# Kernel optimization log

Measured on AMD Instinct MI355X. Metric: run time of the kernel, lower is better.

The kernel has to match this reference:

```python
import jax, jax.numpy as jnp
import numpy as np

HEADS = 16
GN_EPS = 1e-5
NEG = -1e30  # finite stand-in for -inf to keep softmax/vjp NaN-free


def setup_inputs() -> dict:
    key = jax.random.key(0)
    k0, k1, k2, k3 = jax.random.split(key, 4)
    B, C, T = 8, 1024, 1024
    x = jax.random.normal(k0, (B, C, T), dtype=jnp.float32)
    mask = jax.random.randint(k1, (B, T), 0, 2).astype(bool)  # True = masked position
    w_kvq = jax.random.normal(k2, (3 * C, C), dtype=jnp.float32) * 0.02  # Conv1d k=1 == per-time GEMM
    w_out = jax.random.normal(k3, (C, C), dtype=jnp.float32) * 0.02
    gn_weight = jnp.ones((C,), dtype=jnp.float32)
    gn_bias = jnp.zeros((C,), dtype=jnp.float32)
    return {"x": x, "mask": mask, "w_kvq": w_kvq, "w_out": w_out,
            "gn_weight": gn_weight, "gn_bias": gn_bias}


def reference(x, mask, w_kvq, w_out, gn_weight, gn_bias):
    B, C, T = x.shape
    H = HEADS
    d = C // H
    # QKV projection (1x1 conv == GEMM over channels)
    kvq = jnp.einsum('oc,bct->bot', w_kvq, x)  # [B, 3C, T]
    k = kvq[:, :C].reshape(B, H, d, T)
    v = kvq[:, C:2 * C].reshape(B, H, d, T)
    q = kvq[:, 2 * C:].reshape(B, H, d, T)
    scale = 1.0 / np.sqrt(d).astype(np.float32)
    # att[b,h,k,q] = <k_k, q_q> / sqrt(d)
    att = jnp.einsum('bhdk,bhdq->bhkq', k, q) * scale
    # mask key rows, softmax over key axis, then zero masked query columns
    att = jnp.where(mask[:, None, :, None], NEG, att)
    att = jax.nn.softmax(att, axis=2)
    att = jnp.where(mask[:, None, None, :], 0.0, att)
    ctx = jnp.einsum('bhdk,bhkq->bhdq', v, att).reshape(B, C, T)
    out = jnp.einsum('oc,bct->bot', w_out, ctx)
    y = out + x  # residual
    # GroupNorm(1, C): normalize over (C, T) per sample, per-channel affine
    mean = jnp.mean(y, axis=(1, 2), keepdims=True)
    var = jnp.var(y, axis=(1, 2), keepdims=True)
    y = (y - mean) * jax.lax.rsqrt(var + GN_EPS)
    y = y * gn_weight[None, :, None] + gn_bias[None, :, None]
    # torch layout of returned attention: chunks over heads concatenated on batch dim
    att_ret = att.transpose(1, 0, 2, 3).reshape(H * B, T, T)
    return y, att_ret
```

## Files before the change

kernel.cpp:

```cpp
#include <hip/hip_runtime.h>

#define DEVI __device__ __forceinline__

typedef __attribute__((ext_vector_type(8))) short s16x8;
typedef __attribute__((ext_vector_type(4))) float f32x4;
typedef __attribute__((ext_vector_type(4))) unsigned short u16x4;
typedef __attribute__((ext_vector_type(4))) int i32x4;

static constexpr int NB = 8;
static constexpr int NC = 1024;
static constexpr int NT = 1024;
static constexpr int NH = 16;
static constexpr int ND = 64;

DEVI unsigned short cvt_bf16(float f) {
  unsigned int u = __builtin_bit_cast(unsigned int, f);
  u += 0x7fffu + ((u >> 16) & 1u);
  return (unsigned short)(u >> 16);
}

DEVI float fexp2(float x) {
#if __has_builtin(__builtin_amdgcn_exp2f)
  return __builtin_amdgcn_exp2f(x);
#else
  return exp2f(x);
#endif
}

template<int ROWS>
DEVI void stage_tile(const unsigned short* g, int ld, char* lds, int loff, int tid) {
  const int wave = tid >> 6;
  const int lane = tid & 63;
#pragma unroll
  for (int r = 0; r < (ROWS >> 5); ++r) {
    const int row = r * 32 + wave * 8 + (lane >> 3);
    const int c  = lane & 7;
    const int cg = c ^ (row & 7);
    const char* src = (const char*)g + (size_t)row * ld * 2 + cg * 16;
    char* dst = lds + loff + (r * 32 + wave * 8) * 128;
    __builtin_amdgcn_global_load_lds((const __attribute__((address_space(1))) void*)src,
                                     (__attribute__((address_space(3))) void*)dst,
                                     16, 0, 0);
  }
}

DEVI void stage_v(const unsigned short* v, int k0, char* lds, int loff, int tid) {
  const int wave = tid >> 6;
  const int lane = tid & 63;
#pragma unroll
  for (int it = 0; it < 4; ++it) {
    const int d = wave * 16 + it * 4 + (lane >> 4);
    const int c = lane & 15;
    const int cg = c ^ (d & 15);
    const char* src = (const char*)(v + (size_t)d * NT + k0 + cg * 8);
    char* dst = lds + loff + (wave * 16 + it * 4) * 256;
    __builtin_amdgcn_global_load_lds((const __attribute__((address_space(1))) void*)src,
                                     (__attribute__((address_space(3))) void*)dst,
                                     16, 0, 0);
  }
}

DEVI s16x8 frag_ld(const char* lds, int loff, int row, int ks, int lane) {
  const int chunk = (ks * 4 + (lane >> 4)) ^ (row & 7);
  return *(const s16x8*)(lds + loff + row * 128 + chunk * 16);
}

template<int KTOT>
DEVI void gemm_core_128(const unsigned short* A, const unsigned short* Bt,
                        int ldA, int ldB, char* lds, int tid, f32x4 acc[4][4]) {
  const int lane = tid & 63;
  const int wave = tid >> 6;
  const int wr = wave >> 1, wc = wave & 1;
#pragma unroll
  for (int i = 0; i < 4; ++i)
#pragma unroll
    for (int j = 0; j < 4; ++j)
      acc[i][j] = (f32x4){0.f, 0.f, 0.f, 0.f};
  for (int k0 = 0; k0 < KTOT; k0 += 64) {
    __syncthreads();
    stage_tile<128>(A + k0, ldA, lds, 0, tid);
    stage_tile<128>(Bt + k0, ldB, lds, 16384, tid);
    asm volatile("s_waitcnt vmcnt(0)" ::: "memory");
    __syncthreads();
#pragma unroll
    for (int ks = 0; ks < 2; ++ks) {
      s16x8 af[4], bfr[4];
#pragma unroll
      for (int mf = 0; mf < 4; ++mf)
        af[mf] = frag_ld(lds, 0, wr * 64 + mf * 16 + (lane & 15), ks, lane);
#pragma unroll
      for (int nf = 0; nf < 4; ++nf)
        bfr[nf] = frag_ld(lds, 16384, wc * 64 + nf * 16 + (lane & 15), ks, lane);
#pragma unroll
      for (int mf = 0; mf < 4; ++mf)
#pragma unroll
        for (int nf = 0; nf < 4; ++nf)
          acc[mf][nf] = __builtin_amdgcn_mfma_f32_16x16x32_bf16(af[mf], bfr[nf], acc[mf][nf], 0, 0, 0);
    }
  }
}

__global__ __launch_bounds__(256) void k_prep(const float* __restrict__ wkvq,
                                              unsigned short* __restrict__ wkvq_bf,
                                              const float* __restrict__ wout,
                                              unsigned short* __restrict__ wout_bf) {
  const int n1 = 3 * NC * NC / 4, n2 = NC * NC / 4;
  const int stride = gridDim.x * blockDim.x;
  for (int i = blockIdx.x * blockDim.x + threadIdx.x; i < n1 + n2; i += stride) {
    const float* src = (i < n1) ? wkvq + (size_t)i * 4 : wout + (size_t)(i - n1) * 4;
    unsigned short* dst = (i < n1) ? wkvq_bf + (size_t)i * 4 : wout_bf + (size_t)(i - n1) * 4;
    f32x4 v = *(const f32x4*)src;
    u16x4 o;
#pragma unroll
    for (int j = 0; j < 4; ++j) o[j] = cvt_bf16(v[j]);
    *(u16x4*)dst = o;
  }
}

__global__ void k_xT(const float* __restrict__ x, unsigned short* __restrict__ xT) {
  __shared__ float tl[32][33];
  const int bz = blockIdx.z;
  const int t0 = blockIdx.x * 32, c0 = blockIdx.y * 32;
  const int tx = threadIdx.x, ty = threadIdx.y;
#pragma unroll
  for (int j = 0; j < 4; ++j)
    tl[ty + j * 8][tx] = x[((size_t)bz * NC + c0 + ty + j * 8) * NT + t0 + tx];
  __syncthreads();
#pragma unroll
  for (int j = 0; j < 4; ++j)
    xT[((size_t)bz * NT + t0 + ty + j * 8) * NC + c0 + tx] = cvt_bf16(tl[tx][ty + j * 8]);
}

__global__ __launch_bounds__(512, 2) void k_gemm1_256(const unsigned short* __restrict__ W,
                                                      const unsigned short* __restrict__ xT,
                                                      unsigned short* __restrict__ kt,
                                                      unsigned short* __restrict__ qt,
                                                      unsigned short* __restrict__ vbuf) {
  __shared__ char lds[131072];
  const int tid = threadIdx.x, lane = tid & 63, wid = tid >> 6;
  const int wr = wid >> 2, wc = wid & 3;
  const int gid = blockIdx.x;
  const int wg = (gid & 7) * 48 + (gid >> 3);
  const int bn = wg / 12, bm = wg % 12;

  const int r = tid >> 2, ccc = tid & 3;
  const int cg = ccc ^ ((r ^ (r >> 2)) & 3);
  const unsigned short* srcA = W + (size_t)(bm * 256 + r) * NC + cg * 8;
  const unsigned short* srcB = xT + (size_t)(bn * 256 + r) * NC + cg * 8;

  auto stageA = [&](int t) {
    char* d = lds + (t & 3) * 32768 + wid * 1024;
    const unsigned short* s = srcA + t * 32;
    __builtin_amdgcn_global_load_lds((const __attribute__((address_space(1))) void*)s,
                                     (__attribute__((address_space(3))) void*)d, 16, 0, 0);
    __builtin_amdgcn_global_load_lds((const __attribute__((address_space(1))) void*)(s + 128 * NC),
                                     (__attribute__((address_space(3))) void*)(d + 8192), 16, 0, 0);
  };
  auto stageB = [&](int t) {
    char* d = lds + (t & 3) * 32768 + 16384 + wid * 1024;
    const unsigned short* s = srcB + t * 32;
    __builtin_amdgcn_global_load_lds((const __attribute__((address_space(1))) void*)s,
                                     (__attribute__((address_space(3))) void*)d, 16, 0, 0);
    __builtin_amdgcn_global_load_lds((const __attribute__((address_space(1))) void*)(s + 128 * NC),
                                     (__attribute__((address_space(3))) void*)(d + 8192), 16, 0, 0);
  };

  const int l15 = lane & 15, lg = lane >> 4;
  const int rA = wr * 128 + l15;
  const int offA = rA * 64 + (((lg ^ (rA ^ (rA >> 2))) & 3) << 4) + ((lg & ~3) << 4);
  const int rB = wc * 64 + l15;
  const int offB = 16384 + rB * 64 + (((lg ^ (rB ^ (rB >> 2))) & 3) << 4) + ((lg & ~3) << 4);

  f32x4 acc[8][4];
#pragma unroll
  for (int i = 0; i < 8; ++i)
#pragma unroll
    for (int j = 0; j < 4; ++j) acc[i][j] = (f32x4){0.f, 0.f, 0.f, 0.f};

  stageA(0); stageB(0); stageA(1); stageB(1); stageA(2); stageB(2);
  asm volatile("s_waitcnt vmcnt(8)" ::: "memory");
  __builtin_amdgcn_s_barrier();

#pragma unroll
  for (int t = 0; t < 32; ++t) {
    const int slot = (t & 3) * 32768;
    s16x8 af[8], bf[4];
#pragma unroll
    for (int nf = 0; nf < 4; ++nf) bf[nf] = *(const s16x8*)(lds + slot + offB + nf * 1024);
#pragma unroll
    for (int mf = 0; mf < 4; ++mf) af[mf] = *(const s16x8*)(lds + slot + offA + mf * 1024);
    if (t < 29) stageA(t + 3);
    __builtin_amdgcn_s_barrier();
    asm volatile("s_waitcnt lgkmcnt(0)" ::: "memory");
    __builtin_amdgcn_sched_barrier(0);
    __builtin_amdgcn_s_setprio(1);
#pragma unroll
    for (int mf = 0; mf < 4; ++mf)
#pragma unroll
      for (int nf = 0; nf < 4; ++nf)
        acc[mf][nf] = __builtin_amdgcn_mfma_f32_16x16x32_bf16(af[mf], bf[nf], acc[mf][nf], 0, 0, 0);
    __builtin_amdgcn_s_setprio(0);
    __builtin_amdgcn_s_barrier();
#pragma unroll
    for (int mf = 4; mf < 8; ++mf) af[mf] = *(const s16x8*)(lds + slot + offA + mf * 1024);
    if (t < 29) stageB(t + 3);
    if (t < 29)       asm volatile("s_waitcnt vmcnt(8)" ::: "memory");
    else if (t == 29) asm volatile("s_waitcnt vmcnt(4)" ::: "memory");
    else              asm volatile("s_waitcnt vmcnt(0)" ::: "memory");
    __builtin_amdgcn_s_barrier();
    asm volatile("s_waitcnt lgkmcnt(0)" ::: "memory");
    __builtin_amdgcn_sched_barrier(0);
    __builtin_amdgcn_s_setprio(1);
#pragma unroll
    for (int mf = 4; mf < 8; ++mf)
#pragma unroll
      for (int nf = 0; nf < 4; ++nf)
        acc[mf][nf] = __builtin_amdgcn_mfma_f32_16x16x32_bf16(af[mf], bf[nf], acc[mf][nf], 0, 0, 0);
    __builtin_amdgcn_s_setprio(0);
    __builtin_amdgcn_s_barrier();
  }

  const int part = bm >> 2;
  const int d0base = lg << 2;
#pragma unroll
  for (int mf = 0; mf < 8; ++mf) {
    const int h = ((bm & 3) << 2) + (wr << 1) + (mf >> 2);
    const int d0 = ((mf & 3) << 4) + d0base;
#pragma unroll
    for (int nf = 0; nf < 4; ++nf) {
      const int tg = bn * 256 + wc * 64 + nf * 16 + l15;
      const int b = tg >> 10, tt = tg & 1023;
      u16x4 v4;
#pragma unroll
      for (int i = 0; i < 4; ++i) v4[i] = cvt_bf16(acc[mf][nf][i]);
      if (part == 0) {
        *(u16x4*)(kt + (((size_t)(b * NH + h) * NT + tt) * ND + d0)) = v4;
      } else if (part == 1) {
        const size_t basev = ((size_t)(b * NH + h) * ND + d0) * NT + tt;
        vbuf[basev] = v4[0]; vbuf[basev + NT] = v4[1];
        vbuf[basev + 2 * NT] = v4[2]; vbuf[basev + 3 * NT] = v4[3];
      } else {
        *(u16x4*)(qt + (((size_t)(b * NH + h) * NT + tt) * ND + d0)) = v4;
      }
    }
  }
}

__global__ __launch_bounds__(256, 2) void k_att(const unsigned short* __restrict__ kt,
                                                const unsigned short* __restrict__ qt,
                                                const unsigned short* __restrict__ vbuf,
                                                const int* __restrict__ mask,
                                                float* __restrict__ att,
                                                unsigned short* __restrict__ ctxT) {
  __shared__ char lds[81920];
  constexpr int KOFF = 0, QOFF = 16384, VOFF = 32768, POFF = 49152;
  float* colacc = (float*)(lds + POFF);
  unsigned long long* mbits = (unsigned long long*)(lds + POFF + 512);
  const int tid = threadIdx.x, lane = tid & 63, wave = tid >> 6;
  const int wr = wave >> 1, wc = wave & 1;
  const int bh = blockIdx.x, qb = blockIdx.y;
  const int b = bh >> 4, h = bh & 15, hb = h * NB + b;
  const int q0 = qb * 128;
  const unsigned short* ktp = kt + (size_t)bh * NT * ND;
  const unsigned short* qtp = qt + ((size_t)bh * NT + q0) * ND;
  const unsigned short* vp  = vbuf + (size_t)bh * ND * NT;
  const int l15 = lane & 15, g = lane >> 4;

  if (tid < 128) colacc[tid] = 0.f;
  stage_tile<128>(qtp, ND, lds, QOFF, tid);
#pragma unroll
  for (int j = 0; j < 4; ++j) {
    unsigned long long bb = __ballot(mask[b * NT + wave * 256 + j * 64 + lane] != 0);
    if (lane == 0) mbits[wave * 4 + j] = bb;
  }
  i32x4 qm4[4];
#pragma unroll
  for (int nf = 0; nf < 4; ++nf)
    qm4[nf] = *(const i32x4*)(mask + b * NT + q0 + wc * 64 + nf * 16 + g * 4);
  asm volatile("s_waitcnt vmcnt(0)" ::: "memory");
  __syncthreads();

  s16x8 qf[4][2];
#pragma unroll
  for (int nf = 0; nf < 4; ++nf)
#pragma unroll
    for (int ks = 0; ks < 2; ++ks)
      qf[nf][ks] = frag_ld(lds, QOFF, wc * 64 + nf * 16 + l15, ks, lane);

  unsigned int kmask32 = 0;
#pragma unroll
  for (int t = 0; t < 8; ++t) {
    const unsigned long long w64 = mbits[t * 2 + wr];
#pragma unroll
    for (int mf = 0; mf < 4; ++mf)
      kmask32 |= (unsigned int)((w64 >> (mf * 16 + l15)) & 1ull) << (t * 4 + mf);
  }

  const float scl = 0.125f * 1.44269504f;

  f32x4 cs4[4];
#pragma unroll
  for (int nf = 0; nf < 4; ++nf) cs4[nf] = (f32x4){0.f, 0.f, 0.f, 0.f};
  stage_tile<128>(ktp, ND, lds, KOFF, tid);
  for (int t = 0; t < 8; ++t) {
    __builtin_amdgcn_s_barrier();
    if (t < 7) {
      stage_tile<128>(ktp + (size_t)(t + 1) * 128 * ND, ND, lds, (t & 1) ? KOFF : VOFF, tid);
      asm volatile("s_waitcnt vmcnt(4)" ::: "memory");
    } else {
      asm volatile("s_waitcnt vmcnt(0)" ::: "memory");
    }
    __builtin_amdgcn_s_barrier();
    const int koff = (t & 1) ? VOFF : KOFF;
    f32x4 sacc[4][4];
#pragma unroll
    for (int i = 0; i < 4; ++i)
#pragma unroll
      for (int j = 0; j < 4; ++j) sacc[i][j] = (f32x4){0.f, 0.f, 0.f, 0.f};
#pragma unroll
    for (int ks = 0; ks < 2; ++ks) {
      s16x8 kf[4];
#pragma unroll
      for (int mf = 0; mf < 4; ++mf)
        kf[mf] = frag_ld(lds, koff, wr * 64 + mf * 16 + l15, ks, lane);
#pragma unroll
      for (int mf = 0; mf < 4; ++mf)
#pragma unroll
        for (int nf = 0; nf < 4; ++nf)
          sacc[mf][nf] = __builtin_amdgcn_mfma_f32_16x16x32_bf16(qf[nf][ks], kf[mf], sacc[mf][nf], 0, 0, 0);
    }
#pragma unroll
    for (int mf = 0; mf < 4; ++mf) {
      const float kz = ((kmask32 >> (t * 4 + mf)) & 1u) ? 0.f : 1.f;
#pragma unroll
      for (int nf = 0; nf < 4; ++nf)
#pragma unroll
        for (int i = 0; i < 4; ++i)
          cs4[nf][i] += kz * fexp2(sacc[mf][nf][i] * scl);
    }
  }
#pragma unroll
  for (int nf = 0; nf < 4; ++nf)
#pragma unroll
    for (int i = 0; i < 4; ++i) {
      float v = cs4[nf][i];
      v += __shfl_xor(v, 1); v += __shfl_xor(v, 2);
      v += __shfl_xor(v, 4); v += __shfl_xor(v, 8);
      cs4[nf][i] = v;
    }
  if (l15 == 0) {
#pragma unroll
    for (int nf = 0; nf < 4; ++nf)
#pragma unroll
      for (int i = 0; i < 4; ++i)
        atomicAdd(&colacc[wc * 64 + nf * 16 + g * 4 + i], cs4[nf][i]);
  }
  __syncthreads();
  f32x4 sq4[4];
#pragma unroll
  for (int nf = 0; nf < 4; ++nf)
#pragma unroll
    for (int i = 0; i < 4; ++i)
      sq4[nf][i] = qm4[nf][i] ? 0.f : 1.0f / colacc[wc * 64 + nf * 16 + g * 4 + i];

  f32x4 cacc[4][2];
#pragma unroll
  for (int i = 0; i < 4; ++i)
#pragma unroll
    for (int j = 0; j < 2; ++j) cacc[i][j] = (f32x4){0.f, 0.f, 0.f, 0.f};

  stage_tile<128>(ktp, ND, lds, KOFF, tid);
  stage_v(vp, 0, lds, VOFF, tid);
  asm volatile("s_waitcnt vmcnt(0)" ::: "memory");
  __builtin_amdgcn_s_barrier();

  float* attb = att + (size_t)hb * NT * NT + q0 + wc * 64 + g * 4;
  for (int t = 0; t < 8; ++t) {
    f32x4 sacc[4][4];
#pragma unroll
    for (int i = 0; i < 4; ++i)
#pragma unroll
      for (int j = 0; j < 4; ++j) sacc[i][j] = (f32x4){0.f, 0.f, 0.f, 0.f};
#pragma unroll
    for (int ks = 0; ks < 2; ++ks) {
      s16x8 kf[4];
#pragma unroll
      for (int mf = 0; mf < 4; ++mf)
        kf[mf] = frag_ld(lds, KOFF, wr * 64 + mf * 16 + l15, ks, lane);
#pragma unroll
      for (int mf = 0; mf < 4; ++mf)
#pragma unroll
        for (int nf = 0; nf < 4; ++nf)
          sacc[mf][nf] = __builtin_amdgcn_mfma_f32_16x16x32_bf16(qf[nf][ks], kf[mf], sacc[mf][nf], 0, 0, 0);
    }
    __builtin_amdgcn_s_barrier();
    if (t < 7) stage_tile<128>(ktp + (size_t)(t + 1) * 128 * ND, ND, lds, KOFF, tid);
    __builtin_amdgcn_sched_barrier(0);

#pragma unroll
    for (int mf = 0; mf < 4; ++mf) {
      const int kg = t * 128 + wr * 64 + mf * 16 + l15;
      const float kz = ((kmask32 >> (t * 4 + mf)) & 1u) ? 0.f : 1.f;
      const int kloc = wr * 64 + mf * 16 + l15;
#pragma unroll
      for (int nf = 0; nf < 4; ++nf) {
        f32x4 p4;
#pragma unroll
        for (int i = 0; i < 4; ++i)
          p4[i] = kz * fexp2(sacc[mf][nf][i] * scl) * sq4[nf][i];
        __builtin_nontemporal_store(p4, (f32x4*)(attb + (size_t)kg * NT + nf * 16));
        const int qrow = wc * 64 + nf * 16 + g * 4;
#pragma unroll
        for (int i = 0; i < 4; ++i) {
          const int row = qrow + i;
          *(unsigned short*)(lds + POFF + row * 256 + (((kloc >> 3) ^ (row & 15)) << 4)
                             + ((kloc & 7) << 1)) = cvt_bf16(p4[i]);
        }
      }
    }
    asm volatile("s_waitcnt lgkmcnt(0)" ::: "memory");
    __builtin_amdgcn_sched_barrier(0);
    __builtin_amdgcn_s_barrier();
    if (t > 0) {
      if (t < 7) asm volatile("s_waitcnt vmcnt(20)" ::: "memory");
      else       asm volatile("s_waitcnt vmcnt(16)" ::: "memory");
    }

#pragma unroll
    for (int ks2 = 0; ks2 < 4; ++ks2) {
      s16x8 vf[4], pf[2];
      const int chunk = (ks2 << 2) + g;
#pragma unroll
      for (int mf = 0; mf < 4; ++mf) {
        const int d = mf * 16 + l15;
        vf[mf] = *(const s16x8*)(lds + VOFF + d * 256 + ((chunk ^ (d & 15)) << 4));
      }
#pragma unroll
      for (int nf2 = 0; nf2 < 2; ++nf2) {
        const int qloc = wave * 32 + nf2 * 16 + l15;
        pf[nf2] = *(const s16x8*)(lds + POFF + qloc * 256 + ((chunk ^ (qloc & 15)) << 4));
      }
#pragma unroll
      for (int mf = 0; mf < 4; ++mf)
#pragma unroll
        for (int nf2 = 0; nf2 < 2; ++nf2)
          cacc[mf][nf2] = __builtin_amdgcn_mfma_f32_16x16x32_bf16(vf[mf], pf[nf2], cacc[mf][nf2], 0, 0, 0);
    }
    __builtin_amdgcn_s_barrier();
    if (t < 7) {
      stage_v(vp, (t + 1) * 128, lds, VOFF, tid);
      asm volatile("s_waitcnt vmcnt(20)" ::: "memory");
      __builtin_amdgcn_s_barrier();
    }
  }

#pragma unroll
  for (int mf = 0; mf < 4; ++mf) {
    const int d0 = mf * 16 + (g << 2);
#pragma unroll
    for (int nf2 = 0; nf2 < 2; ++nf2) {
      const int q = q0 + wave * 32 + nf2 * 16 + l15;
      u16x4 v4;
#pragma unroll
      for (int i = 0; i < 4; ++i) v4[i] = cvt_bf16(cacc[mf][nf2][i]);
      *(u16x4*)(ctxT + ((size_t)b * NT + q) * NC + h * ND + d0) = v4;
    }
  }
}

__global__ __launch_bounds__(256) void k_outgemm(const unsigned short* __restrict__ Wo,
                                                 const unsigned short* __restrict__ ctxT,
                                                 const float* __restrict__ x,
                                                 float* __restrict__ y0,
                                                 float* __restrict__ partials) {
  __shared__ char lds[32832];
  const int tid = threadIdx.x, lane = tid & 63, wave = tid >> 6;
  const int wr = wave >> 1, wc = wave & 1;
  const int bm = blockIdx.x, bn = blockIdx.y, b = blockIdx.z;
  const unsigned short* A = Wo + (size_t)bm * 128 * NC;
  const unsigned short* Bt = ctxT + ((size_t)b * NT + (size_t)bn * 128) * NC;
  f32x4 acc[4][4];
  gemm_core_128<NC>(A, Bt, NC, NC, lds, tid, acc);

  float lsum = 0.f, lsq = 0.f;
#pragma unroll
  for (int mf = 0; mf < 4; ++mf) {
#pragma unroll
    for (int nf = 0; nf < 4; ++nf) {
      const int gc = bn * 128 + wc * 64 + nf * 16 + (lane & 15);
#pragma unroll
      for (int i = 0; i < 4; ++i) {
        const int gr = bm * 128 + wr * 64 + mf * 16 + ((lane >> 4) << 2) + i;
        const size_t idx = ((size_t)b * NC + gr) * NT + gc;
        const float v = acc[mf][nf][i] + x[idx];
        y0[idx] = v;
        lsum += v; lsq += v * v;
      }
    }
  }
#pragma unroll
  for (int off = 32; off; off >>= 1) {
    lsum += __shfl_xor(lsum, off);
    lsq += __shfl_xor(lsq, off);
  }
  __syncthreads();
  float* red = (float*)(lds + 32768);
  if (lane == 0) { red[wave * 2] = lsum; red[wave * 2 + 1] = lsq; }
  __syncthreads();
  if (tid == 0) {
    const float s = red[0] + red[2] + red[4] + red[6];
    const float qq = red[1] + red[3] + red[5] + red[7];
    const int bi = bm * 8 + bn;
    partials[((size_t)b * 64 + bi) * 2] = s;
    partials[((size_t)b * 64 + bi) * 2 + 1] = qq;
  }
}

__global__ void k_gnstats(const float* __restrict__ partials, float* __restrict__ gnp) {
  const int b = blockIdx.x, t = threadIdx.x;
  float s = partials[((size_t)b * 64 + t) * 2];
  float q = partials[((size_t)b * 64 + t) * 2 + 1];
#pragma unroll
  for (int off = 32; off; off >>= 1) {
    s += __shfl_xor(s, off);
    q += __shfl_xor(q, off);
  }
  if (t == 0) {
    const float n = 1048576.f;
    const float mean = s / n;
    const float var = q / n - mean * mean;
    gnp[b * 2] = mean;
    gnp[b * 2 + 1] = rsqrtf(var + 1e-5f);
  }
}

__global__ __launch_bounds__(256) void k_gnapply(const float* __restrict__ y0,
                                                 const float* __restrict__ gnp,
                                                 const float* __restrict__ gw,
                                                 const float* __restrict__ gb,
                                                 float* __restrict__ out) {
  const size_t n4 = (size_t)NB * NC * NT / 4;
  const size_t stride = (size_t)gridDim.x * blockDim.x;
  for (size_t i = (size_t)blockIdx.x * blockDim.x + threadIdx.x; i < n4; i += stride) {
    const size_t base = i * 4;
    const int b = (int)(base >> 20);
    const int c = (int)((base >> 10) & 1023);
    const f32x4 v = *(const f32x4*)(y0 + base);
    const float m = gnp[b * 2], r = gnp[b * 2 + 1];
    const float sw = gw[c] * r, sb = gb[c];
    f32x4 o;
#pragma unroll
    for (int j = 0; j < 4; ++j) o[j] = (v[j] - m) * sw + sb;
    *(f32x4*)(out + base) = o;
  }
}

extern "C" void kernel_launch(void* const* d_in, const int* in_sizes, int n_in,
                              void* d_out, int out_size, void* d_ws, size_t ws_size,
                              hipStream_t stream) {
  (void)in_sizes; (void)n_in; (void)out_size; (void)ws_size;
  const float* x     = (const float*)d_in[0];
  const int*   mask  = (const int*)d_in[1];
  const float* w_kvq = (const float*)d_in[2];
  const float* w_out = (const float*)d_in[3];
  const float* gnw   = (const float*)d_in[4];
  const float* gnb   = (const float*)d_in[5];
  float* outy = (float*)d_out;
  float* att  = outy + (size_t)NB * NC * NT;

  char* ws = (char*)d_ws;
  unsigned short* wkvq_bf = (unsigned short*)(ws);
  unsigned short* wout_bf = (unsigned short*)(ws + 6291456);
  unsigned short* xT      = (unsigned short*)(ws + 8388608);
  unsigned short* ctxT    = xT;
  unsigned short* kt      = (unsigned short*)(ws + 25165824);
  unsigned short* qt      = (unsigned short*)(ws + 41943040);
  float*          y0      = (float*)(ws + 25165824);
  unsigned short* vbuf    = (unsigned short*)(ws + 58720256);
  float*          part    = (float*)(ws + 76021760);
  float*          gnp     = (float*)(ws + 76025856);

  k_prep<<<2048, 256, 0, stream>>>(w_kvq, wkvq_bf, w_out, wout_bf);
  k_xT<<<dim3(32, 32, 8), dim3(32, 8), 0, stream>>>(x, xT);
  k_gemm1_256<<<384, 512, 0, stream>>>(wkvq_bf, xT, kt, qt, vbuf);
  k_att<<<dim3(128, 8), 256, 0, stream>>>(kt, qt, vbuf, mask, att, ctxT);
  k_outgemm<<<dim3(8, 8, 8), 256, 0, stream>>>(wout_bf, ctxT, x, y0, part);
  k_gnstats<<<8, 64, 0, stream>>>(part, gnp);
  k_gnapply<<<4096, 256, 0, stream>>>(y0, gnp, gnw, gnb, outy);
}
```

Measured before the change: 346.6 us.

## Single-pass attention: cache unnormalized probabilities in registers, normalize afterward

The attention kernel previously made two passes over K: one to compute column softmax sums and another to recompute QK^T, normalize, write the attention matrix and accumulate P·V. It now makes one pass that computes exp scores, accumulates column sums, stores unnormalized bf16 probabilities in registers and LDS, and accumulates P·V immediately. Normalization is applied afterward to the context and to the cached probabilities written to the attention output. Blocks go from 256 to 512 threads with double-buffered K/V staging, which raises register pressure (64 u16x4 cached per thread) and rounds the stored attention values through bf16.

```diff
diff --git a/kernel.cpp b/kernel.cpp
--- a/kernel.cpp
+++ b/kernel.cpp
@@ -17,6 +17,11 @@
   unsigned int u = __builtin_bit_cast(unsigned int, f);
   u += 0x7fffu + ((u >> 16) & 1u);
   return (unsigned short)(u >> 16);
+}
+
+DEVI float bf16_to_f32(unsigned short s) {
+  unsigned int u = (unsigned int)s << 16;
+  return __builtin_bit_cast(float, u);
 }
 
 DEVI float fexp2(float x) {
@@ -44,16 +49,27 @@
   }
 }
 
-DEVI void stage_v(const unsigned short* v, int k0, char* lds, int loff, int tid) {
-  const int wave = tid >> 6;
-  const int lane = tid & 63;
-#pragma unroll
-  for (int it = 0; it < 4; ++it) {
-    const int d = wave * 16 + it * 4 + (lane >> 4);
-    const int c = lane & 15;
-    const int cg = c ^ (d & 15);
+DEVI void stage_k512(const unsigned short* g, char* lds, int loff, int tid) {
+  const int wave = tid >> 6, lane = tid & 63;
+#pragma unroll
+  for (int r = 0; r < 2; ++r) {
+    const int row = r * 64 + wave * 8 + (lane >> 3);
+    const int c = lane & 7, cg = c ^ (row & 7);
+    const char* src = (const char*)g + (size_t)row * 128 + cg * 16;
+    char* dst = lds + loff + (r * 64 + wave * 8) * 128;
+    __builtin_amdgcn_global_load_lds((const __attribute__((address_space(1))) void*)src,
+                                     (__attribute__((address_space(3))) void*)dst,
+                                     16, 0, 0);
+  }
+}
+DEVI void stage_v512(const unsigned short* v, int k0, char* lds, int loff, int tid) {
+  const int wave = tid >> 6, lane = tid & 63;
+#pragma unroll
+  for (int r = 0; r < 2; ++r) {
+    const int d = r * 32 + wave * 4 + (lane >> 4);
+    const int c = lane & 15, cg = c ^ (d & 15);
     const char* src = (const char*)(v + (size_t)d * NT + k0 + cg * 8);
-    char* dst = lds + loff + (wave * 16 + it * 4) * 256;
+    char* dst = lds + loff + (r * 32 + wave * 4) * 256;
     __builtin_amdgcn_global_load_lds((const __attribute__((address_space(1))) void*)src,
                                      (__attribute__((address_space(3))) void*)dst,
                                      16, 0, 0);
@@ -246,18 +262,19 @@
   }
 }
 
-__global__ __launch_bounds__(256, 2) void k_att(const unsigned short* __restrict__ kt,
-                                                const unsigned short* __restrict__ qt,
-                                                const unsigned short* __restrict__ vbuf,
-                                                const int* __restrict__ mask,
-                                                float* __restrict__ att,
-                                                unsigned short* __restrict__ ctxT) {
-  __shared__ char lds[81920];
-  constexpr int KOFF = 0, QOFF = 16384, VOFF = 32768, POFF = 49152;
-  float* colacc = (float*)(lds + POFF);
-  unsigned long long* mbits = (unsigned long long*)(lds + POFF + 512);
-  const int tid = threadIdx.x, lane = tid & 63, wave = tid >> 6;
-  const int wr = wave >> 1, wc = wave & 1;
+__global__ __launch_bounds__(512, 1) void k_att2(const unsigned short* __restrict__ kt,
+                                                 const unsigned short* __restrict__ qt,
+                                                 const unsigned short* __restrict__ vbuf,
+                                                 const int* __restrict__ mask,
+                                                 float* __restrict__ att,
+                                                 unsigned short* __restrict__ ctxT) {
+  __shared__ char lds[115456];
+  constexpr int QOFF = 0, KOFF0 = 16384, KOFF1 = 32768, VOFF0 = 49152, VOFF1 = 65536;
+  constexpr int POFF = 81920, COFF = 114688;
+  float* colacc = (float*)(lds + COFF);
+  unsigned long long* mbits = (unsigned long long*)(lds + COFF + 512);
+  const int tid = threadIdx.x, lane = tid & 63, wid = tid >> 6;
+  const int wr = wid >> 2, wc = wid & 3;
   const int bh = blockIdx.x, qb = blockIdx.y;
   const int b = bh >> 4, h = bh & 15, hb = h * NB + b;
   const int q0 = qb * 128;
@@ -267,25 +284,27 @@
   const int l15 = lane & 15, g = lane >> 4;
 
   if (tid < 128) colacc[tid] = 0.f;
-  stage_tile<128>(qtp, ND, lds, QOFF, tid);
-#pragma unroll
-  for (int j = 0; j < 4; ++j) {
-    unsigned long long bb = __ballot(mask[b * NT + wave * 256 + j * 64 + lane] != 0);
-    if (lane == 0) mbits[wave * 4 + j] = bb;
-  }
-  i32x4 qm4[4];
-#pragma unroll
-  for (int nf = 0; nf < 4; ++nf)
-    qm4[nf] = *(const i32x4*)(mask + b * NT + q0 + wc * 64 + nf * 16 + g * 4);
+  stage_k512(qtp, lds, QOFF, tid);
+  stage_k512(ktp, lds, KOFF0, tid);
+  stage_v512(vp, 0, lds, VOFF0, tid);
+#pragma unroll
+  for (int j = 0; j < 2; ++j) {
+    unsigned long long bb = __ballot(mask[b * NT + wid * 128 + j * 64 + lane] != 0);
+    if (lane == 0) mbits[wid * 2 + j] = bb;
+  }
+  i32x4 qm4[2];
+#pragma unroll
+  for (int nf = 0; nf < 2; ++nf)
+    qm4[nf] = *(const i32x4*)(mask + b * NT + q0 + wc * 32 + nf * 16 + g * 4);
   asm volatile("s_waitcnt vmcnt(0)" ::: "memory");
   __syncthreads();
 
-  s16x8 qf[4][2];
-#pragma unroll
-  for (int nf = 0; nf < 4; ++nf)
+  s16x8 qf[2][2];
+#pragma unroll
+  for (int nf = 0; nf < 2; ++nf)
 #pragma unroll
     for (int ks = 0; ks < 2; ++ks)
-      qf[nf][ks] = frag_ld(lds, QOFF, wc * 64 + nf * 16 + l15, ks, lane);
+      qf[nf][ks] = frag_ld(lds, QOFF, wc * 32 + nf * 16 + l15, ks, lane);
 
   unsigned int kmask32 = 0;
 #pragma unroll
@@ -297,26 +316,31 @@
   }
 
   const float scl = 0.125f * 1.44269504f;
-
-  f32x4 cs4[4];
-#pragma unroll
-  for (int nf = 0; nf < 4; ++nf) cs4[nf] = (f32x4){0.f, 0.f, 0.f, 0.f};
-  stage_tile<128>(ktp, ND, lds, KOFF, tid);
+  u16x4 preg[8][8];
+  f32x4 cs4[2] = {(f32x4){0.f,0.f,0.f,0.f}, (f32x4){0.f,0.f,0.f,0.f}};
+  f32x4 cacc[4];
+#pragma unroll
+  for (int i = 0; i < 4; ++i) cacc[i] = (f32x4){0.f, 0.f, 0.f, 0.f};
+
+#pragma unroll
   for (int t = 0; t < 8; ++t) {
-    __builtin_amdgcn_s_barrier();
+    if (t > 0) __builtin_amdgcn_s_barrier();
     if (t < 7) {
-      stage_tile<128>(ktp + (size_t)(t + 1) * 128 * ND, ND, lds, (t & 1) ? KOFF : VOFF, tid);
+      stage_k512(ktp + (size_t)(t + 1) * 128 * ND, lds, (t & 1) ? KOFF0 : KOFF1, tid);
+      stage_v512(vp, (t + 1) * 128, lds, (t & 1) ? VOFF0 : VOFF1, tid);
       asm volatile("s_waitcnt vmcnt(4)" ::: "memory");
     } else {
       asm volatile("s_waitcnt vmcnt(0)" ::: "memory");
     }
     __builtin_amdgcn_s_barrier();
-    const int koff = (t & 1) ? VOFF : KOFF;
-    f32x4 sacc[4][4];
+    const int koff = (t & 1) ? KOFF1 : KOFF0;
+    const int voff = (t & 1) ? VOFF1 : VOFF0;
+
+    f32x4 sacc[4][2];
 #pragma unroll
     for (int i = 0; i < 4; ++i)
 #pragma unroll
-      for (int j = 0; j < 4; ++j) sacc[i][j] = (f32x4){0.f, 0.f, 0.f, 0.f};
+      for (int j = 0; j < 2; ++j) sacc[i][j] = (f32x4){0.f, 0.f, 0.f, 0.f};
 #pragma unroll
     for (int ks = 0; ks < 2; ++ks) {
       s16x8 kf[4];
@@ -326,21 +350,58 @@
 #pragma unroll
       for (int mf = 0; mf < 4; ++mf)
 #pragma unroll
-        for (int nf = 0; nf < 4; ++nf)
+        for (int nf = 0; nf < 2; ++nf)
           sacc[mf][nf] = __builtin_amdgcn_mfma_f32_16x16x32_bf16(qf[nf][ks], kf[mf], sacc[mf][nf], 0, 0, 0);
     }
+
 #pragma unroll
     for (int mf = 0; mf < 4; ++mf) {
       const float kz = ((kmask32 >> (t * 4 + mf)) & 1u) ? 0.f : 1.f;
-#pragma unroll
-      for (int nf = 0; nf < 4; ++nf)
-#pragma unroll
-        for (int i = 0; i < 4; ++i)
-          cs4[nf][i] += kz * fexp2(sacc[mf][nf][i] * scl);
-    }
-  }
-#pragma unroll
-  for (int nf = 0; nf < 4; ++nf)
+      const int kloc = wr * 64 + mf * 16 + l15;
+#pragma unroll
+      for (int nf = 0; nf < 2; ++nf) {
+        f32x4 p;
+#pragma unroll
+        for (int i = 0; i < 4; ++i) {
+          p[i] = kz * fexp2(sacc[mf][nf][i] * scl);
+          cs4[nf][i] += p[i];
+        }
+        u16x4 pr;
+#pragma unroll
+        for (int i = 0; i < 4; ++i) pr[i] = cvt_bf16(p[i]);
+        preg[t][mf * 2 + nf] = pr;
+        const int qrow = wc * 32 + nf * 16 + g * 4;
+#pragma unroll
+        for (int i = 0; i < 4; ++i) {
+          const int row = qrow + i;
+          *(unsigned short*)(lds + POFF + row * 256 + (((kloc >> 3) ^ (row & 15)) << 4)
+                             + ((kloc & 7) << 1)) = pr[i];
+        }
+      }
+    }
+    asm volatile("s_waitcnt lgkmcnt(0)" ::: "memory");
+    __builtin_amdgcn_sched_barrier(0);
+    __builtin_amdgcn_s_barrier();
+
+#pragma unroll
+    for (int ks2 = 0; ks2 < 4; ++ks2) {
+      const int chunk = (ks2 << 2) + g;
+      s16x8 vf[4];
+#pragma unroll
+      for (int mf = 0; mf < 4; ++mf) {
+        const int d = mf * 16 + l15;
+        vf[mf] = *(const s16x8*)(lds + voff + d * 256 + ((chunk ^ (d & 15)) << 4));
+      }
+      const int qloc = wid * 16 + l15;
+      s16x8 pf = *(const s16x8*)(lds + POFF + qloc * 256 + ((chunk ^ (qloc & 15)) << 4));
+#pragma unroll
+      for (int mf = 0; mf < 4; ++mf)
+        cacc[mf] = __builtin_amdgcn_mfma_f32_16x16x32_bf16(vf[mf], pf, cacc[mf], 0, 0, 0);
+    }
+  }
+
+#pragma unroll
+  for (int nf = 0; nf < 2; ++nf)
 #pragma unroll
     for (int i = 0; i < 4; ++i) {
       float v = cs4[nf][i];
@@ -350,120 +411,45 @@
     }
   if (l15 == 0) {
 #pragma unroll
-    for (int nf = 0; nf < 4; ++nf)
+    for (int nf = 0; nf < 2; ++nf)
 #pragma unroll
       for (int i = 0; i < 4; ++i)
-        atomicAdd(&colacc[wc * 64 + nf * 16 + g * 4 + i], cs4[nf][i]);
+        atomicAdd(&colacc[wc * 32 + nf * 16 + g * 4 + i], cs4[nf][i]);
   }
   __syncthreads();
-  f32x4 sq4[4];
-#pragma unroll
-  for (int nf = 0; nf < 4; ++nf)
+  f32x4 sq4[2];
+#pragma unroll
+  for (int nf = 0; nf < 2; ++nf)
 #pragma unroll
     for (int i = 0; i < 4; ++i)
-      sq4[nf][i] = qm4[nf][i] ? 0.f : 1.0f / colacc[wc * 64 + nf * 16 + g * 4 + i];
-
-  f32x4 cacc[4][2];
-#pragma unroll
-  for (int i = 0; i < 4; ++i)
-#pragma unroll
-    for (int j = 0; j < 2; ++j) cacc[i][j] = (f32x4){0.f, 0.f, 0.f, 0.f};
-
-  stage_tile<128>(ktp, ND, lds, KOFF, tid);
-  stage_v(vp, 0, lds, VOFF, tid);
-  asm volatile("s_waitcnt vmcnt(0)" ::: "memory");
-  __builtin_amdgcn_s_barrier();
-
-  float* attb = att + (size_t)hb * NT * NT + q0 + wc * 64 + g * 4;
+      sq4[nf][i] = qm4[nf][i] ? 0.f : 1.0f / colacc[wc * 32 + nf * 16 + g * 4 + i];
+
+  {
+    const int qe = wid * 16 + l15;
+    const float sqe = mask[b * NT + q0 + qe] ? 0.f : 1.0f / colacc[qe];
+#pragma unroll
+    for (int mf = 0; mf < 4; ++mf) {
+      u16x4 v4;
+#pragma unroll
+      for (int i = 0; i < 4; ++i) v4[i] = cvt_bf16(cacc[mf][i] * sqe);
+      *(u16x4*)(ctxT + ((size_t)b * NT + q0 + qe) * NC + h * ND + mf * 16 + g * 4) = v4;
+    }
+  }
+
+  float* attb = att + (size_t)hb * NT * NT + q0 + wc * 32 + g * 4;
+#pragma unroll
   for (int t = 0; t < 8; ++t) {
-    f32x4 sacc[4][4];
-#pragma unroll
-    for (int i = 0; i < 4; ++i)
-#pragma unroll
-      for (int j = 0; j < 4; ++j) sacc[i][j] = (f32x4){0.f, 0.f, 0.f, 0.f};
-#pragma unroll
-    for (int ks = 0; ks < 2; ++ks) {
-      s16x8 kf[4];
-#pragma unroll
-      for (int mf = 0; mf < 4; ++mf)
-        kf[mf] = frag_ld(lds, KOFF, wr * 64 + mf * 16 + l15, ks, lane);
-#pragma unroll
-      for (int mf = 0; mf < 4; ++mf)
-#pragma unroll
-        for (int nf = 0; nf < 4; ++nf)
-          sacc[mf][nf] = __builtin_amdgcn_mfma_f32_16x16x32_bf16(qf[nf][ks], kf[mf], sacc[mf][nf], 0, 0, 0);
-    }
-    __builtin_amdgcn_s_barrier();
-    if (t < 7) stage_tile<128>(ktp + (size_t)(t + 1) * 128 * ND, ND, lds, KOFF, tid);
-    __builtin_amdgcn_sched_barrier(0);
-
 #pragma unroll
     for (int mf = 0; mf < 4; ++mf) {
       const int kg = t * 128 + wr * 64 + mf * 16 + l15;
-      const float kz = ((kmask32 >> (t * 4 + mf)) & 1u) ? 0.f : 1.f;
-      const int kloc = wr * 64 + mf * 16 + l15;
-#pragma unroll
-      for (int nf = 0; nf < 4; ++nf) {
+#pragma unroll
+      for (int nf = 0; nf < 2; ++nf) {
+        const u16x4 pr = preg[t][mf * 2 + nf];
         f32x4 p4;
 #pragma unroll
-        for (int i = 0; i < 4; ++i)
-          p4[i] = kz * fexp2(sacc[mf][nf][i] * scl) * sq4[nf][i];
+        for (int i = 0; i < 4; ++i) p4[i] = bf16_to_f32(pr[i]) * sq4[nf][i];
         __builtin_nontemporal_store(p4, (f32x4*)(attb + (size_t)kg * NT + nf * 16));
-        const int qrow = wc * 64 + nf * 16 + g * 4;
-#pragma unroll
-        for (int i = 0; i < 4; ++i) {
-          const int row = qrow + i;
-          *(unsigned short*)(lds + POFF + row * 256 + (((kloc >> 3) ^ (row & 15)) << 4)
-                             + ((kloc & 7) << 1)) = cvt_bf16(p4[i]);
-        }
       }
-    }
-    asm volatile("s_waitcnt lgkmcnt(0)" ::: "memory");
-    __builtin_amdgcn_sched_barrier(0);
-    __builtin_amdgcn_s_barrier();
-    if (t > 0) {
-      if (t < 7) asm volatile("s_waitcnt vmcnt(20)" ::: "memory");
-      else       asm volatile("s_waitcnt vmcnt(16)" ::: "memory");
-    }
-
-#pragma unroll
-    for (int ks2 = 0; ks2 < 4; ++ks2) {
-      s16x8 vf[4], pf[2];
-      const int chunk = (ks2 << 2) + g;
-#pragma unroll
-      for (int mf = 0; mf < 4; ++mf) {
-        const int d = mf * 16 + l15;
-        vf[mf] = *(const s16x8*)(lds + VOFF + d * 256 + ((chunk ^ (d & 15)) << 4));
-      }
-#pragma unroll
-      for (int nf2 = 0; nf2 < 2; ++nf2) {
-        const int qloc = wave * 32 + nf2 * 16 + l15;
-        pf[nf2] = *(const s16x8*)(lds + POFF + qloc * 256 + ((chunk ^ (qloc & 15)) << 4));
-      }
-#pragma unroll
-      for (int mf = 0; mf < 4; ++mf)
-#pragma unroll
-        for (int nf2 = 0; nf2 < 2; ++nf2)
-          cacc[mf][nf2] = __builtin_amdgcn_mfma_f32_16x16x32_bf16(vf[mf], pf[nf2], cacc[mf][nf2], 0, 0, 0);
-    }
-    __builtin_amdgcn_s_barrier();
-    if (t < 7) {
-      stage_v(vp, (t + 1) * 128, lds, VOFF, tid);
-      asm volatile("s_waitcnt vmcnt(20)" ::: "memory");
-      __builtin_amdgcn_s_barrier();
-    }
-  }
-
-#pragma unroll
-  for (int mf = 0; mf < 4; ++mf) {
-    const int d0 = mf * 16 + (g << 2);
-#pragma unroll
-    for (int nf2 = 0; nf2 < 2; ++nf2) {
-      const int q = q0 + wave * 32 + nf2 * 16 + l15;
-      u16x4 v4;
-#pragma unroll
-      for (int i = 0; i < 4; ++i) v4[i] = cvt_bf16(cacc[mf][nf2][i]);
-      *(u16x4*)(ctxT + ((size_t)b * NT + q) * NC + h * ND + d0) = v4;
     }
   }
 }
@@ -583,7 +569,7 @@
   k_prep<<<2048, 256, 0, stream>>>(w_kvq, wkvq_bf, w_out, wout_bf);
   k_xT<<<dim3(32, 32, 8), dim3(32, 8), 0, stream>>>(x, xT);
   k_gemm1_256<<<384, 512, 0, stream>>>(wkvq_bf, xT, kt, qt, vbuf);
-  k_att<<<dim3(128, 8), 256, 0, stream>>>(kt, qt, vbuf, mask, att, ctxT);
+  k_att2<<<dim3(128, 8), 512, 0, stream>>>(kt, qt, vbuf, mask, att, ctxT);
   k_outgemm<<<dim3(8, 8, 8), 256, 0, stream>>>(wout_bf, ctxT, x, y0, part);
   k_gnstats<<<8, 64, 0, stream>>>(part, gnp);
   k_gnapply<<<4096, 256, 0, stream>>>(y0, gnp, gnw, gnb, outy);
```

New measurement: 414.6 us. 19.6% more time.

## Halve key tile to 64 and shrink LDS to raise attention occupancy

Applied to the files above, without the earlier changes.

Cuts the key/value tile per iteration from 128 to 64 keys, so the K, V and P buffers in LDS shrink and the Q staging area is reused for P. Total LDS drops from 80 KB to about 33 KB and launch bounds go from 2 to 3 blocks per CU, aiming to hide the latency of the large attention-matrix stores. V staging now uses the generic tile loader, and the vmcnt waits are retuned for the smaller tiles. In exchange there are twice as many loop iterations and barriers, and less MFMA work between each sync.

```diff
diff --git a/kernel.cpp b/kernel.cpp
--- a/kernel.cpp
+++ b/kernel.cpp
@@ -38,22 +38,6 @@
     const int cg = c ^ (row & 7);
     const char* src = (const char*)g + (size_t)row * ld * 2 + cg * 16;
     char* dst = lds + loff + (r * 32 + wave * 8) * 128;
-    __builtin_amdgcn_global_load_lds((const __attribute__((address_space(1))) void*)src,
-                                     (__attribute__((address_space(3))) void*)dst,
-                                     16, 0, 0);
-  }
-}
-
-DEVI void stage_v(const unsigned short* v, int k0, char* lds, int loff, int tid) {
-  const int wave = tid >> 6;
-  const int lane = tid & 63;
-#pragma unroll
-  for (int it = 0; it < 4; ++it) {
-    const int d = wave * 16 + it * 4 + (lane >> 4);
-    const int c = lane & 15;
-    const int cg = c ^ (d & 15);
-    const char* src = (const char*)(v + (size_t)d * NT + k0 + cg * 8);
-    char* dst = lds + loff + (wave * 16 + it * 4) * 256;
     __builtin_amdgcn_global_load_lds((const __attribute__((address_space(1))) void*)src,
                                      (__attribute__((address_space(3))) void*)dst,
                                      16, 0, 0);
@@ -246,16 +230,16 @@
   }
 }
 
-__global__ __launch_bounds__(256, 2) void k_att(const unsigned short* __restrict__ kt,
+__global__ __launch_bounds__(256, 3) void k_att(const unsigned short* __restrict__ kt,
                                                 const unsigned short* __restrict__ qt,
                                                 const unsigned short* __restrict__ vbuf,
                                                 const int* __restrict__ mask,
                                                 float* __restrict__ att,
                                                 unsigned short* __restrict__ ctxT) {
-  __shared__ char lds[81920];
-  constexpr int KOFF = 0, QOFF = 16384, VOFF = 32768, POFF = 49152;
-  float* colacc = (float*)(lds + POFF);
-  unsigned long long* mbits = (unsigned long long*)(lds + POFF + 512);
+  __shared__ char lds[33408];
+  constexpr int KOFF = 0, VOFF = 8192, POFF = 16384, COFF = 32768;
+  float* colacc = (float*)(lds + COFF);
+  unsigned long long* mbits = (unsigned long long*)(lds + COFF + 512);
   const int tid = threadIdx.x, lane = tid & 63, wave = tid >> 6;
   const int wr = wave >> 1, wc = wave & 1;
   const int bh = blockIdx.x, qb = blockIdx.y;
@@ -267,7 +251,7 @@
   const int l15 = lane & 15, g = lane >> 4;
 
   if (tid < 128) colacc[tid] = 0.f;
-  stage_tile<128>(qtp, ND, lds, QOFF, tid);
+  stage_tile<128>(qtp, ND, lds, POFF, tid);
 #pragma unroll
   for (int j = 0; j < 4; ++j) {
     unsigned long long bb = __ballot(mask[b * NT + wave * 256 + j * 64 + lane] != 0);
@@ -285,15 +269,16 @@
   for (int nf = 0; nf < 4; ++nf)
 #pragma unroll
     for (int ks = 0; ks < 2; ++ks)
-      qf[nf][ks] = frag_ld(lds, QOFF, wc * 64 + nf * 16 + l15, ks, lane);
+      qf[nf][ks] = frag_ld(lds, POFF, wc * 64 + nf * 16 + l15, ks, lane);
+  __syncthreads();
 
   unsigned int kmask32 = 0;
 #pragma unroll
-  for (int t = 0; t < 8; ++t) {
-    const unsigned long long w64 = mbits[t * 2 + wr];
-#pragma unroll
-    for (int mf = 0; mf < 4; ++mf)
-      kmask32 |= (unsigned int)((w64 >> (mf * 16 + l15)) & 1ull) << (t * 4 + mf);
+  for (int t = 0; t < 16; ++t) {
+    const unsigned long long w64 = mbits[t];
+#pragma unroll
+    for (int mf = 0; mf < 2; ++mf)
+      kmask32 |= (unsigned int)((w64 >> (wr * 32 + mf * 16 + l15)) & 1ull) << (t * 2 + mf);
   }
 
   const float scl = 0.125f * 1.44269504f;
@@ -301,37 +286,37 @@
   f32x4 cs4[4];
 #pragma unroll
   for (int nf = 0; nf < 4; ++nf) cs4[nf] = (f32x4){0.f, 0.f, 0.f, 0.f};
-  stage_tile<128>(ktp, ND, lds, KOFF, tid);
-  for (int t = 0; t < 8; ++t) {
-    __builtin_amdgcn_s_barrier();
-    if (t < 7) {
-      stage_tile<128>(ktp + (size_t)(t + 1) * 128 * ND, ND, lds, (t & 1) ? KOFF : VOFF, tid);
-      asm volatile("s_waitcnt vmcnt(4)" ::: "memory");
+  stage_tile<64>(ktp, ND, lds, KOFF, tid);
+  for (int t = 0; t < 16; ++t) {
+    __builtin_amdgcn_s_barrier();
+    if (t < 15) {
+      stage_tile<64>(ktp + (size_t)(t + 1) * 64 * ND, ND, lds, (t & 1) ? KOFF : VOFF, tid);
+      asm volatile("s_waitcnt vmcnt(2)" ::: "memory");
     } else {
       asm volatile("s_waitcnt vmcnt(0)" ::: "memory");
     }
     __builtin_amdgcn_s_barrier();
     const int koff = (t & 1) ? VOFF : KOFF;
-    f32x4 sacc[4][4];
-#pragma unroll
-    for (int i = 0; i < 4; ++i)
+    f32x4 sacc[2][4];
+#pragma unroll
+    for (int i = 0; i < 2; ++i)
 #pragma unroll
       for (int j = 0; j < 4; ++j) sacc[i][j] = (f32x4){0.f, 0.f, 0.f, 0.f};
 #pragma unroll
     for (int ks = 0; ks < 2; ++ks) {
-      s16x8 kf[4];
-#pragma unroll
-      for (int mf = 0; mf < 4; ++mf)
-        kf[mf] = frag_ld(lds, koff, wr * 64 + mf * 16 + l15, ks, lane);
-#pragma unroll
-      for (int mf = 0; mf < 4; ++mf)
+      s16x8 kf[2];
+#pragma unroll
+      for (int mf = 0; mf < 2; ++mf)
+        kf[mf] = frag_ld(lds, koff, wr * 32 + mf * 16 + l15, ks, lane);
+#pragma unroll
+      for (int mf = 0; mf < 2; ++mf)
 #pragma unroll
         for (int nf = 0; nf < 4; ++nf)
           sacc[mf][nf] = __builtin_amdgcn_mfma_f32_16x16x32_bf16(qf[nf][ks], kf[mf], sacc[mf][nf], 0, 0, 0);
     }
 #pragma unroll
-    for (int mf = 0; mf < 4; ++mf) {
-      const float kz = ((kmask32 >> (t * 4 + mf)) & 1u) ? 0.f : 1.f;
+    for (int mf = 0; mf < 2; ++mf) {
+      const float kz = ((kmask32 >> (t * 2 + mf)) & 1u) ? 0.f : 1.f;
 #pragma unroll
       for (int nf = 0; nf < 4; ++nf)
 #pragma unroll
@@ -369,39 +354,39 @@
 #pragma unroll
     for (int j = 0; j < 2; ++j) cacc[i][j] = (f32x4){0.f, 0.f, 0.f, 0.f};
 
-  stage_tile<128>(ktp, ND, lds, KOFF, tid);
-  stage_v(vp, 0, lds, VOFF, tid);
+  stage_tile<64>(ktp, ND, lds, KOFF, tid);
+  stage_tile<64>(vp, NT, lds, VOFF, tid);
   asm volatile("s_waitcnt vmcnt(0)" ::: "memory");
   __builtin_amdgcn_s_barrier();
 
   float* attb = att + (size_t)hb * NT * NT + q0 + wc * 64 + g * 4;
-  for (int t = 0; t < 8; ++t) {
-    f32x4 sacc[4][4];
-#pragma unroll
-    for (int i = 0; i < 4; ++i)
+  for (int t = 0; t < 16; ++t) {
+    f32x4 sacc[2][4];
+#pragma unroll
+    for (int i = 0; i < 2; ++i)
 #pragma unroll
       for (int j = 0; j < 4; ++j) sacc[i][j] = (f32x4){0.f, 0.f, 0.f, 0.f};
 #pragma unroll
     for (int ks = 0; ks < 2; ++ks) {
-      s16x8 kf[4];
-#pragma unroll
-      for (int mf = 0; mf < 4; ++mf)
-        kf[mf] = frag_ld(lds, KOFF, wr * 64 + mf * 16 + l15, ks, lane);
-#pragma unroll
-      for (int mf = 0; mf < 4; ++mf)
+      s16x8 kf[2];
+#pragma unroll
+      for (int mf = 0; mf < 2; ++mf)
+        kf[mf] = frag_ld(lds, KOFF, wr * 32 + mf * 16 + l15, ks, lane);
+#pragma unroll
+      for (int mf = 0; mf < 2; ++mf)
 #pragma unroll
         for (int nf = 0; nf < 4; ++nf)
           sacc[mf][nf] = __builtin_amdgcn_mfma_f32_16x16x32_bf16(qf[nf][ks], kf[mf], sacc[mf][nf], 0, 0, 0);
     }
     __builtin_amdgcn_s_barrier();
-    if (t < 7) stage_tile<128>(ktp + (size_t)(t + 1) * 128 * ND, ND, lds, KOFF, tid);
+    if (t < 15) stage_tile<64>(ktp + (size_t)(t + 1) * 64 * ND, ND, lds, KOFF, tid);
     __builtin_amdgcn_sched_barrier(0);
 
 #pragma unroll
-    for (int mf = 0; mf < 4; ++mf) {
-      const int kg = t * 128 + wr * 64 + mf * 16 + l15;
-      const float kz = ((kmask32 >> (t * 4 + mf)) & 1u) ? 0.f : 1.f;
-      const int kloc = wr * 64 + mf * 16 + l15;
+    for (int mf = 0; mf < 2; ++mf) {
+      const int kg = t * 64 + wr * 32 + mf * 16 + l15;
+      const float kz = ((kmask32 >> (t * 2 + mf)) & 1u) ? 0.f : 1.f;
+      const int kloc = wr * 32 + mf * 16 + l15;
 #pragma unroll
       for (int nf = 0; nf < 4; ++nf) {
         f32x4 p4;
@@ -413,7 +398,7 @@
 #pragma unroll
         for (int i = 0; i < 4; ++i) {
           const int row = qrow + i;
-          *(unsigned short*)(lds + POFF + row * 256 + (((kloc >> 3) ^ (row & 15)) << 4)
+          *(unsigned short*)(lds + POFF + row * 128 + (((kloc >> 3) ^ (row & 7)) << 4)
                              + ((kloc & 7) << 1)) = cvt_bf16(p4[i]);
         }
       }
@@ -421,25 +406,18 @@
     asm volatile("s_waitcnt lgkmcnt(0)" ::: "memory");
     __builtin_amdgcn_sched_barrier(0);
     __builtin_amdgcn_s_barrier();
-    if (t > 0) {
-      if (t < 7) asm volatile("s_waitcnt vmcnt(20)" ::: "memory");
-      else       asm volatile("s_waitcnt vmcnt(16)" ::: "memory");
-    }
-
-#pragma unroll
-    for (int ks2 = 0; ks2 < 4; ++ks2) {
+    if (t < 15) asm volatile("s_waitcnt vmcnt(10)" ::: "memory");
+    else        asm volatile("s_waitcnt vmcnt(8)" ::: "memory");
+
+#pragma unroll
+    for (int ks2 = 0; ks2 < 2; ++ks2) {
       s16x8 vf[4], pf[2];
-      const int chunk = (ks2 << 2) + g;
-#pragma unroll
-      for (int mf = 0; mf < 4; ++mf) {
-        const int d = mf * 16 + l15;
-        vf[mf] = *(const s16x8*)(lds + VOFF + d * 256 + ((chunk ^ (d & 15)) << 4));
-      }
-#pragma unroll
-      for (int nf2 = 0; nf2 < 2; ++nf2) {
-        const int qloc = wave * 32 + nf2 * 16 + l15;
-        pf[nf2] = *(const s16x8*)(lds + POFF + qloc * 256 + ((chunk ^ (qloc & 15)) << 4));
-      }
+#pragma unroll
+      for (int mf = 0; mf < 4; ++mf)
+        vf[mf] = frag_ld(lds, VOFF, mf * 16 + l15, ks2, lane);
+#pragma unroll
+      for (int nf2 = 0; nf2 < 2; ++nf2)
+        pf[nf2] = frag_ld(lds, POFF, wave * 32 + nf2 * 16 + l15, ks2, lane);
 #pragma unroll
       for (int mf = 0; mf < 4; ++mf)
 #pragma unroll
@@ -447,9 +425,9 @@
           cacc[mf][nf2] = __builtin_amdgcn_mfma_f32_16x16x32_bf16(vf[mf], pf[nf2], cacc[mf][nf2], 0, 0, 0);
     }
     __builtin_amdgcn_s_barrier();
-    if (t < 7) {
-      stage_v(vp, (t + 1) * 128, lds, VOFF, tid);
-      asm volatile("s_waitcnt vmcnt(20)" ::: "memory");
+    if (t < 15) {
+      stage_tile<64>(vp + (t + 1) * 64, NT, lds, VOFF, tid);
+      asm volatile("s_waitcnt vmcnt(10)" ::: "memory");
       __builtin_amdgcn_s_barrier();
     }
   }
```

Measured after the change: 344.0 us. About the same (-0.7%).
